# Optimization experiments

Hardware: AMD Instinct MI355X
Metric: run time of the kernel (lower is better)

The kernel has to match this reference:

```python
import jax, jax.numpy as jnp
import numpy as np

T, R, I = 16384, 1024, 128   # time steps, reservoir size, input size
CONN, SR = 0.05, 0.9         # connectivity_rate, spectral_radius


def _make_reservoir(rng):
    # Faithful to ESN.create_reservoir_weights: uniform[0,1), sparsify by
    # connectivity_rate, rescale to target spectral radius, flip half the
    # entries' signs.
    W = rng.random((R, R)).astype(np.float32)
    W[rng.random((R, R)) > CONN] = 0.0
    cur_sr = np.max(np.abs(np.linalg.eigvals(W)))
    W = W * (SR / cur_sr)
    neg = rng.choice(R * R, (R * R) // 2, replace=False)
    Wf = W.reshape(-1).copy()
    Wf[neg] *= -1.0
    return Wf.reshape(R, R).astype(np.float32)


def setup_inputs() -> dict:
    rng = np.random.default_rng(0)
    W_res = jnp.asarray(_make_reservoir(rng))
    key = jax.random.key(0)
    k1, k2 = jax.random.split(key)
    X = jax.random.normal(k1, (T, I), dtype=jnp.float32)
    # nn.init.uniform_(w, a=-1, b=1)
    W_in = jax.random.uniform(k2, (R, I), dtype=jnp.float32, minval=-1.0, maxval=1.0)
    state0 = jnp.zeros((R,), dtype=jnp.float32)
    return {"X": X, "W_in": W_in, "W_res": W_res, "state0": state0}


def reference(X, W_in, W_res, state0):
    # state_t = tanh(W_in @ x_t + W_res @ state_{t-1}); collect all states (T, R).
    # Input projections are independent across time -> one big GEMM up front.
    U = X @ W_in.T  # (T, R)

    def step(s, u):
        s = jnp.tanh(u + W_res @ s)
        return s, s

    _, all_states = jax.lax.scan(step, state0, U)
    return all_states  # (T, R), matches update_state's all_states
```

## Files before the change

kernel.cpp:

```cpp
#include <hip/hip_runtime.h>
#include <hip/hip_bf16.h>
#include <stdint.h>


constexpr int T_N = 16384;
constexpr int R_N = 1024;
constexpr int I_N = 128;

constexpr int BT = 64, BR = 64;

__global__ __launch_bounds__(256) void gemm_u_kernel(
    const float* __restrict__ X, const float* __restrict__ Win,
    float* __restrict__ U)
{
    __shared__ float XS[BT][68];
    __shared__ float WS[BR][68];
    const int tid = threadIdx.x;
    const int ty = tid >> 4, tx = tid & 15;
    const int t0 = blockIdx.x * BT;
    const int r0 = blockIdx.y * BR;
    float acc[4][4] = {};

    for (int k0 = 0; k0 < I_N; k0 += 64) {
        for (int idx = tid; idx < BT * 16; idx += 256) {
            int row = idx >> 4, c4 = (idx & 15) << 2;
            *reinterpret_cast<float4*>(&XS[row][c4]) =
                *reinterpret_cast<const float4*>(&X[(size_t)(t0 + row) * I_N + k0 + c4]);
        }
        for (int idx = tid; idx < BR * 16; idx += 256) {
            int row = idx >> 4, c4 = (idx & 15) << 2;
            *reinterpret_cast<float4*>(&WS[row][c4]) =
                *reinterpret_cast<const float4*>(&Win[(size_t)(r0 + row) * I_N + k0 + c4]);
        }
        __syncthreads();
#pragma unroll
        for (int k = 0; k < 64; k += 4) {
            float4 a[4], b[4];
#pragma unroll
            for (int i = 0; i < 4; ++i)
                a[i] = *reinterpret_cast<const float4*>(&XS[ty + 16 * i][k]);
#pragma unroll
            for (int jj = 0; jj < 4; ++jj)
                b[jj] = *reinterpret_cast<const float4*>(&WS[tx + 16 * jj][k]);
#pragma unroll
            for (int i = 0; i < 4; ++i)
#pragma unroll
                for (int jj = 0; jj < 4; ++jj)
                    acc[i][jj] += a[i].x * b[jj].x + a[i].y * b[jj].y +
                                  a[i].z * b[jj].z + a[i].w * b[jj].w;
        }
        __syncthreads();
    }
#pragma unroll
    for (int i = 0; i < 4; ++i)
#pragma unroll
        for (int jj = 0; jj < 4; ++jj)
            U[(size_t)(t0 + ty + 16 * i) * R_N + (r0 + tx + 16 * jj)] = acc[i][jj];
}

constexpr int GBLK = 16;
constexpr int B2   = 512;
constexpr int RPB  = R_N / GBLK;
constexpr int TPR  = B2 / RPB;
constexpr int KMAX = 96;
constexpr int NSL  = KMAX / TPR;

__device__ __forceinline__ float fast_tanh(float x) {
    float ax = fabsf(x);
    float e  = __expf(-2.0f * ax);
    float y  = (1.0f - e) / (1.0f + e);
    return copysignf(y, x);
}

__global__ __launch_bounds__(512) void esn_scan_kernel(
    const float* __restrict__ Wres, const float* __restrict__ state0,
    float* out, unsigned long long* ws)
{
    __shared__ float sbuf[2][R_N];
    __shared__ uint2 ell[RPB][KMAX];
    __shared__ int   cnt[RPB];

    const int tid  = threadIdx.x;
    const int b    = blockIdx.x;
    const int row0 = b * RPB;

    if (tid < RPB) cnt[tid] = 0;
    __syncthreads();
    for (int idx = tid; idx < RPB * R_N; idx += B2) {
        int r = idx >> 10, c = idx & (R_N - 1);
        float w = Wres[(size_t)(row0 + r) * R_N + c];
        if (w != 0.0f) {
            int slot = atomicAdd(&cnt[r], 1);
            if (slot < KMAX) ell[r][slot] = make_uint2((uint32_t)c, __float_as_uint(w));
        }
    }
    __syncthreads();

    const int rloc = tid / TPR;
    const int j    = tid % TPR;
    const int row  = row0 + rloc;
    int   cols[NSL];
    float vals[NSL];
    {
        int myn = cnt[rloc];
#pragma unroll
        for (int k = 0; k < NSL; ++k) {
            int slot = j + k * TPR;
            if (slot < myn) {
                uint2 e = ell[rloc][slot];
                cols[k] = (int)e.x;
                vals[k] = __uint_as_float(e.y);
            } else { cols[k] = 0; vals[k] = 0.0f; }
        }
    }

    const int i0 = tid, i1 = tid + B2;
    sbuf[0][i0] = state0[i0];
    sbuf[0][i1] = state0[i1];

    for (int t = 0; t < T_N; ++t) {
        const int p = t & 1;

        float uval = (j == 0) ? out[(size_t)t * R_N + row] : 0.0f;

        if (t > 0) {
            const unsigned long long* src = ws + (size_t)((t - 1) & 1) * R_N;
            const uint32_t want = (uint32_t)t;
            unsigned long long w0 = 0, w1 = 0;
            bool ok0 = false, ok1 = false;
            do {
                if (!ok0) {
                    w0 = __hip_atomic_load(&src[i0], __ATOMIC_RELAXED,
                                           __HIP_MEMORY_SCOPE_AGENT);
                    ok0 = (uint32_t)(w0 >> 32) >= want;
                }
                if (!ok1) {
                    w1 = __hip_atomic_load(&src[i1], __ATOMIC_RELAXED,
                                           __HIP_MEMORY_SCOPE_AGENT);
                    ok1 = (uint32_t)(w1 >> 32) >= want;
                }
            } while (!(ok0 && ok1));
            sbuf[p][i0] = __uint_as_float((uint32_t)w0);
            sbuf[p][i1] = __uint_as_float((uint32_t)w1);
        }
        __syncthreads();

        float acc = 0.0f;
#pragma unroll
        for (int k = 0; k < NSL; ++k) acc += vals[k] * sbuf[p][cols[k]];

        acc += __shfl_xor(acc, 1, TPR);
        acc += __shfl_xor(acc, 2, TPR);
        acc += __shfl_xor(acc, 4, TPR);

        if (j == 0) {
            float y = fast_tanh(uval + acc);
            out[(size_t)t * R_N + row] = y;
            unsigned long long pkt =
                ((unsigned long long)(uint32_t)(t + 1) << 32) | __float_as_uint(y);
            __hip_atomic_store(&ws[(size_t)p * R_N + row], pkt,
                               __ATOMIC_RELAXED, __HIP_MEMORY_SCOPE_AGENT);
        }
    }
}

extern "C" void kernel_launch(void* const* d_in, const int* in_sizes, int n_in,
                              void* d_out, int out_size, void* d_ws, size_t ws_size,
                              hipStream_t stream)
{
    const float* X      = (const float*)d_in[0];
    const float* W_in   = (const float*)d_in[1];
    const float* W_res  = (const float*)d_in[2];
    const float* state0 = (const float*)d_in[3];
    float* out = (float*)d_out;
    unsigned long long* ws = (unsigned long long*)d_ws;

    hipMemsetAsync(d_ws, 0, 2 * R_N * sizeof(unsigned long long), stream);

    dim3 g1(T_N / BT, R_N / BR);
    gemm_u_kernel<<<g1, 256, 0, stream>>>(X, W_in, out);

    esn_scan_kernel<<<GBLK, B2, 0, stream>>>(W_res, state0, out, ws);
}
```

Measured before the change: 25.71 ms.

## Halve scan blocks to 8 with 1024 threads and prefetch next input

Cuts the persistent scan grid from 16 to 8 blocks of 1024 threads, so each thread polls a single flag slot per step and fewer blocks take part in the cross-block handoff. It prefetches the next step's input projection a step early and publishes the state packet before the plain output store. It also adds a bounded spin count as a deadlock guard. In exchange each block holds twice the rows in its LDS ELL table, and the capped spin could read a stale value if a producer stalls long enough.

Result: faster. 24.27 ms (-5.6%).

```diff
diff --git a/kernel.cpp b/kernel.cpp
--- a/kernel.cpp
+++ b/kernel.cpp
@@ -58,12 +58,16 @@
             U[(size_t)(t0 + ty + 16 * i) * R_N + (r0 + tx + 16 * jj)] = acc[i][jj];
 }
 
-constexpr int GBLK = 16;
-constexpr int B2   = 512;
-constexpr int RPB  = R_N / GBLK;
-constexpr int TPR  = B2 / RPB;
-constexpr int KMAX = 96;
-constexpr int NSL  = KMAX / TPR;
+constexpr int GBLK  = 8;
+constexpr int B2    = 1024;
+constexpr int RPB   = R_N / GBLK;
+constexpr int TPR   = 8;
+constexpr int KMAX  = 96;
+constexpr int NSL   = KMAX / TPR;
+constexpr int DEPTH = 2;
+constexpr int PCAP  = 1 << 20;
+
+typedef unsigned long long ull;
 
 __device__ __forceinline__ float fast_tanh(float x) {
     float ax = fabsf(x);
@@ -72,11 +76,11 @@
     return copysignf(y, x);
 }
 
-__global__ __launch_bounds__(512) void esn_scan_kernel(
+__global__ __launch_bounds__(1024) void esn_scan_kernel(
     const float* __restrict__ Wres, const float* __restrict__ state0,
-    float* out, unsigned long long* ws)
+    float* out, ull* slots)
 {
-    __shared__ float sbuf[2][R_N];
+    __shared__ float sbuf[DEPTH][R_N];
     __shared__ uint2 ell[RPB][KMAX];
     __shared__ int   cnt[RPB];
 
@@ -114,34 +118,27 @@
         }
     }
 
-    const int i0 = tid, i1 = tid + B2;
-    sbuf[0][i0] = state0[i0];
-    sbuf[0][i1] = state0[i1];
+    sbuf[1][tid] = state0[tid];
+
+    float u_cur = (j == 0) ? out[row] : 0.0f;
+    __syncthreads();
 
     for (int t = 0; t < T_N; ++t) {
-        const int p = t & 1;
+        const int p = (t - 1) & 1;
 
-        float uval = (j == 0) ? out[(size_t)t * R_N + row] : 0.0f;
+        float u_next = 0.0f;
+        if (j == 0 && t + 1 < T_N) u_next = out[(size_t)(t + 1) * R_N + row];
 
         if (t > 0) {
-            const unsigned long long* src = ws + (size_t)((t - 1) & 1) * R_N;
+            const ull* addr = slots + ((size_t)p << 10) + tid;
             const uint32_t want = (uint32_t)t;
-            unsigned long long w0 = 0, w1 = 0;
-            bool ok0 = false, ok1 = false;
+            ull w;
+            int rounds = 0;
             do {
-                if (!ok0) {
-                    w0 = __hip_atomic_load(&src[i0], __ATOMIC_RELAXED,
-                                           __HIP_MEMORY_SCOPE_AGENT);
-                    ok0 = (uint32_t)(w0 >> 32) >= want;
-                }
-                if (!ok1) {
-                    w1 = __hip_atomic_load(&src[i1], __ATOMIC_RELAXED,
-                                           __HIP_MEMORY_SCOPE_AGENT);
-                    ok1 = (uint32_t)(w1 >> 32) >= want;
-                }
-            } while (!(ok0 && ok1));
-            sbuf[p][i0] = __uint_as_float((uint32_t)w0);
-            sbuf[p][i1] = __uint_as_float((uint32_t)w1);
+                w = __hip_atomic_load(addr, __ATOMIC_RELAXED,
+                                      __HIP_MEMORY_SCOPE_AGENT);
+            } while ((uint32_t)(w >> 32) < want && ++rounds < PCAP);
+            sbuf[p][tid] = __uint_as_float((uint32_t)w);
         }
         __syncthreads();
 
@@ -154,13 +151,13 @@
         acc += __shfl_xor(acc, 4, TPR);
 
         if (j == 0) {
-            float y = fast_tanh(uval + acc);
+            float y = fast_tanh(u_cur + acc);
+            ull pkt = ((ull)(uint32_t)(t + 1) << 32) | (ull)__float_as_uint(y);
+            __hip_atomic_store(&slots[((size_t)(t & 1) << 10) + row], pkt,
+                               __ATOMIC_RELAXED, __HIP_MEMORY_SCOPE_AGENT);
             out[(size_t)t * R_N + row] = y;
-            unsigned long long pkt =
-                ((unsigned long long)(uint32_t)(t + 1) << 32) | __float_as_uint(y);
-            __hip_atomic_store(&ws[(size_t)p * R_N + row], pkt,
-                               __ATOMIC_RELAXED, __HIP_MEMORY_SCOPE_AGENT);
         }
+        u_cur = u_next;
     }
 }
 
@@ -173,12 +170,12 @@
     const float* W_res  = (const float*)d_in[2];
     const float* state0 = (const float*)d_in[3];
     float* out = (float*)d_out;
-    unsigned long long* ws = (unsigned long long*)d_ws;
+    ull* slots = (ull*)d_ws;
 
-    hipMemsetAsync(d_ws, 0, 2 * R_N * sizeof(unsigned long long), stream);
+    hipMemsetAsync(d_ws, 0, (size_t)DEPTH * R_N * sizeof(ull), stream);
 
     dim3 g1(T_N / BT, R_N / BR);
     gemm_u_kernel<<<g1, 256, 0, stream>>>(X, W_in, out);
 
-    esn_scan_kernel<<<GBLK, B2, 0, stream>>>(W_res, state0, out, ws);
+    esn_scan_kernel<<<GBLK, B2, 0, stream>>>(W_res, state0, out, slots);
 }
```
